# Kernel optimization log

Hardware: AMD Instinct MI355X
Metric: run time of the kernel (lower is better)

## Reference

```python
import jax, jax.numpy as jnp
import numpy as np

B, T, D, H = 2, 2048, 1024, 16
DH = D // H


def setup_inputs() -> dict:
    key = jax.random.key(0)
    ks = jax.random.split(key, 11)
    s = 1.0 / np.sqrt(D)
    return {
        "q": jax.random.normal(ks[0], (B, T, D), jnp.float32),
        "k": jax.random.normal(ks[1], (B, T, D), jnp.float32),
        "v": jax.random.normal(ks[2], (B, T, D), jnp.float32),
        "wq_w": jax.random.normal(ks[3], (D, D), jnp.float32) * s,
        "wq_b": jnp.zeros((D,), jnp.float32),
        "wk_w": jax.random.normal(ks[4], (D, D), jnp.float32) * s,
        "wk_b": jnp.zeros((D,), jnp.float32),
        "wv_w": jax.random.normal(ks[5], (D, D), jnp.float32) * s,
        "wv_b": jnp.zeros((D,), jnp.float32),
        "wo_w": jax.random.normal(ks[6], (D, D), jnp.float32) * s,
        "wo_b": jnp.zeros((D,), jnp.float32),
    }


def reference(q, k, v, wq_w, wq_b, wk_w, wk_b, wv_w, wv_b, wo_w, wo_b):
    b, t, d = q.shape
    # Linear projections (torch Linear: x @ W^T + b)
    wq = (q @ wq_w.T + wq_b).reshape(b, t, H, DH)
    wk = (k @ wk_w.T + wk_b).reshape(b, t, H, DH)
    wv = (v @ wv_w.T + wv_b).reshape(b, t, H, DH)
    # scaled dot-product attention: [b,h,t,s]
    scores = jnp.einsum('bthd,bshd->bhts', wq, wk) / jnp.sqrt(jnp.float32(DH))
    probs = jax.nn.softmax(scores, axis=-1)
    attn = jnp.einsum('bhts,bshd->bthd', probs, wv)  # [b,t,h,dh]
    attn = attn.reshape(b, t, d)
    return attn @ wo_w.T + wo_b
```

## Files before the change

kernel.cpp:

```cpp
#include <hip/hip_runtime.h>
#include <hip/hip_bf16.h>
#include <stdint.h>

#define Bn  2
#define Tn  2048
#define Dn  1024
#define Hn  16
#define DHn 64
#define Mn  (Bn*Tn)

typedef __attribute__((ext_vector_type(8))) short short8;
typedef __attribute__((ext_vector_type(4))) short short4v;
typedef __attribute__((ext_vector_type(4))) float f32x4;

__device__ __forceinline__ f32x4 fzero4() { f32x4 z = {0.f, 0.f, 0.f, 0.f}; return z; }

#define TR16(dst, a32) asm volatile("ds_read_b64_tr_b16 %0, %1" : "=v"(dst) : "v"(a32))
#define EXP2(x) __builtin_amdgcn_exp2f(x)

__device__ __forceinline__ short8 cvt8(const float4& a, const float4& b) {
    union { __hip_bfloat16 h[8]; short8 u; } w;
    w.h[0] = __float2bfloat16(a.x); w.h[1] = __float2bfloat16(a.y);
    w.h[2] = __float2bfloat16(a.z); w.h[3] = __float2bfloat16(a.w);
    w.h[4] = __float2bfloat16(b.x); w.h[5] = __float2bfloat16(b.y);
    w.h[6] = __float2bfloat16(b.z); w.h[7] = __float2bfloat16(b.w);
    return w.u;
}

__global__ void cvt3_kernel(const float* __restrict__ a0, const float* __restrict__ a1,
                            const float* __restrict__ a2,
                            __hip_bfloat16* __restrict__ o0, __hip_bfloat16* __restrict__ o1,
                            __hip_bfloat16* __restrict__ o2, int n)
{
    const int i = (blockIdx.x * blockDim.x + threadIdx.x) * 8;
    if (i >= n) return;
    const float* in = blockIdx.y == 0 ? a0 : (blockIdx.y == 1 ? a1 : a2);
    __hip_bfloat16* out = blockIdx.y == 0 ? o0 : (blockIdx.y == 1 ? o1 : o2);
    float4 a = *(const float4*)(in + i);
    float4 b = *(const float4*)(in + i + 4);
    *(short8*)(out + i) = cvt8(a, b);
}

__global__ __launch_bounds__(256, 3)
void gemm_qkv_kernel(const float* __restrict__ qa, const float* __restrict__ ka,
                     const float* __restrict__ va,
                     const __hip_bfloat16* __restrict__ wq, const __hip_bfloat16* __restrict__ wk,
                     const __hip_bfloat16* __restrict__ wv,
                     const float* __restrict__ bq_, const float* __restrict__ bk_,
                     const float* __restrict__ bv_,
                     __hip_bfloat16* __restrict__ Qp, __hip_bfloat16* __restrict__ Kp,
                     __hip_bfloat16* __restrict__ Vp)
{
    __shared__ alignas(16) short As[2][128*32];
    __shared__ alignas(16) short Bs[2][128*32];
    const int grp = blockIdx.y >> 3;
    const float* A           = grp == 0 ? qa : (grp == 1 ? ka : va);
    const __hip_bfloat16* Bw = grp == 0 ? wq : (grp == 1 ? wk : wv);
    const float* bias        = grp == 0 ? bq_ : (grp == 1 ? bk_ : bv_);
    __hip_bfloat16* C        = grp == 0 ? Qp : (grp == 1 ? Kp : Vp);
    const float scl          = grp == 0 ? 0.18033688011112042f : 1.0f;

    const int t = threadIdx.x, lane = t & 63, wave = t >> 6;
    const int wm = wave >> 1, wn = wave & 1;
    const int row0 = blockIdx.x * 128, col0 = (blockIdx.y & 7) * 128;

    f32x4 acc[4][4];
#pragma unroll
    for (int m = 0; m < 4; ++m)
#pragma unroll
        for (int n = 0; n < 4; ++n) acc[m][n] = fzero4();

    const int srow = wave*16 + (lane >> 2);
    const int skk  = (lane & 3) * 8;
    const int ldsb = wave * 1024 + (lane & 63) * 16;

    float4 ra[2][2];
    auto LOAD_A = [&](int k0) {
#pragma unroll
        for (int i = 0; i < 2; ++i) {
            const float* ap = A + (size_t)(row0 + i*64 + srow)*Dn + k0 + skk;
            ra[i][0] = *(const float4*)ap;
            ra[i][1] = *(const float4*)(ap + 4);
        }
    };
    auto WRITE_A = [&](int buf) {
#pragma unroll
        for (int i = 0; i < 2; ++i)
            *(short8*)((char*)As[buf] + i*4096 + ldsb) = cvt8(ra[i][0], ra[i][1]);
    };
    auto STAGE_B = [&](int buf, int k0) {
#pragma unroll
        for (int i = 0; i < 2; ++i)
            __builtin_amdgcn_global_load_lds(
                (const __attribute__((address_space(1))) void*)(Bw + (size_t)(col0 + i*64 + srow)*Dn + k0 + skk),
                (__attribute__((address_space(3))) void*)((char*)Bs[buf] + i*4096 + wave*1024 + (lane&63)*16), 16, 0, 0);
    };

    LOAD_A(0);
    STAGE_B(0, 0);
    WRITE_A(0);
    __syncthreads();
    int cur = 0;
    for (int k0 = 0; k0 < Dn; k0 += 32) {
        const bool more = (k0 + 32 < Dn);
        if (more) { LOAD_A(k0 + 32); STAGE_B(cur ^ 1, k0 + 32); }
        short8 af[4], bf_[4];
#pragma unroll
        for (int m = 0; m < 4; ++m)
            af[m] = *(const short8*)((char*)As[cur] + (wm*64 + m*16 + (lane & 15))*64 + (lane >> 4)*16);
#pragma unroll
        for (int n = 0; n < 4; ++n)
            bf_[n] = *(const short8*)((char*)Bs[cur] + (wn*64 + n*16 + (lane & 15))*64 + (lane >> 4)*16);
        __builtin_amdgcn_s_setprio(1);
#pragma unroll
        for (int m = 0; m < 4; ++m)
#pragma unroll
            for (int n = 0; n < 4; ++n)
                acc[m][n] = __builtin_amdgcn_mfma_f32_16x16x32_bf16(af[m], bf_[n], acc[m][n], 0, 0, 0);
        __builtin_amdgcn_s_setprio(0);
        __builtin_amdgcn_sched_barrier(0);
        if (more) WRITE_A(cur ^ 1);
        __syncthreads();
        cur ^= 1;
    }

#pragma unroll
    for (int n = 0; n < 4; ++n) {
        const int col = col0 + wn*64 + n*16 + (lane & 15);
        const float bv = bias[col];
#pragma unroll
        for (int m = 0; m < 4; ++m) {
            const int rb_ = row0 + wm*64 + m*16 + (lane>>4)*4;
#pragma unroll
            for (int i = 0; i < 4; ++i)
                C[(size_t)(rb_+i)*Dn + col] = __float2bfloat16((acc[m][n][i] + bv) * scl);
        }
    }
}

__global__ __launch_bounds__(256, 4)
void gemm_out_kernel(const __hip_bfloat16* __restrict__ A,
                     const __hip_bfloat16* __restrict__ Bw,
                     const float* __restrict__ bias,
                     float* __restrict__ C)
{
    __shared__ alignas(16) short As[2][64*32];
    __shared__ alignas(16) short Bs[2][128*32];
    const int t = threadIdx.x, lane = t & 63, wave = t >> 6;
    const int wm = wave >> 1, wn = wave & 1;
    const int row0 = blockIdx.x * 64, col0 = blockIdx.y * 128;

    f32x4 acc[2][4];
#pragma unroll
    for (int m = 0; m < 2; ++m)
#pragma unroll
        for (int n = 0; n < 4; ++n) acc[m][n] = fzero4();

    const int srow = wave*16 + (lane >> 2);
    const int skk  = (lane & 3) * 8;
    const int ldsb = wave * 1024;

    auto STAGE = [&](int buf, int k0) {
        __builtin_amdgcn_global_load_lds(
            (const __attribute__((address_space(1))) void*)(A + (size_t)(row0 + srow)*Dn + k0 + skk),
            (__attribute__((address_space(3))) void*)((char*)As[buf] + ldsb), 16, 0, 0);
#pragma unroll
        for (int i = 0; i < 2; ++i)
            __builtin_amdgcn_global_load_lds(
                (const __attribute__((address_space(1))) void*)(Bw + (size_t)(col0 + i*64 + srow)*Dn + k0 + skk),
                (__attribute__((address_space(3))) void*)((char*)Bs[buf] + i*4096 + ldsb), 16, 0, 0);
    };

    STAGE(0, 0);
    __syncthreads();
    int cur = 0;
    for (int k0 = 0; k0 < Dn; k0 += 32) {
        if (k0 + 32 < Dn) STAGE(cur ^ 1, k0 + 32);
        short8 af[2], bf_[4];
#pragma unroll
        for (int m = 0; m < 2; ++m)
            af[m] = *(const short8*)((char*)As[cur] + (wm*32 + m*16 + (lane & 15))*64 + (lane >> 4)*16);
#pragma unroll
        for (int n = 0; n < 4; ++n)
            bf_[n] = *(const short8*)((char*)Bs[cur] + (wn*64 + n*16 + (lane & 15))*64 + (lane >> 4)*16);
        __builtin_amdgcn_s_setprio(1);
#pragma unroll
        for (int m = 0; m < 2; ++m)
#pragma unroll
            for (int n = 0; n < 4; ++n)
                acc[m][n] = __builtin_amdgcn_mfma_f32_16x16x32_bf16(af[m], bf_[n], acc[m][n], 0, 0, 0);
        __builtin_amdgcn_s_setprio(0);
        __syncthreads();
        cur ^= 1;
    }

#pragma unroll
    for (int n = 0; n < 4; ++n) {
        const int col = col0 + wn*64 + n*16 + (lane & 15);
        const float bv = bias[col];
#pragma unroll
        for (int m = 0; m < 2; ++m) {
            const int rb_ = row0 + wm*32 + m*16 + (lane>>4)*4;
#pragma unroll
            for (int i = 0; i < 4; ++i)
                C[(size_t)(rb_+i)*Dn + col] = acc[m][n][i] + bv;
        }
    }
}

#define VPL 1288

__global__ __launch_bounds__(256, 2)
void attn_kernel(const __hip_bfloat16* __restrict__ Q,
                 const __hip_bfloat16* __restrict__ K,
                 const __hip_bfloat16* __restrict__ V,
                 __hip_bfloat16* __restrict__ O,
                 const float* __restrict__ wo_src,
                 __hip_bfloat16* __restrict__ wo_dst)
{
    __shared__ alignas(16) short Vlds[2*2*4*VPL];
    const int t = threadIdx.x, lane = t & 63, wave = t >> 6;

    {
        const int off = (blockIdx.x * 256 + t) * 8;
        float4 a = *(const float4*)(wo_src + off);
        float4 b2 = *(const float4*)(wo_src + off + 4);
        *(short8*)(wo_dst + off) = cvt8(a, b2);
    }

    const int g = lane >> 4, c = lane & 15;
    const int pk = wave & 1, qh = wave >> 1;
    const int blk = (blockIdx.x & 7) * 64 + (blockIdx.x >> 3);
    const int qb = blk & 15;
    const int h  = (blk >> 4) & (Hn - 1);
    const int b  = blk >> 8;
    const size_t base = (size_t)b * Tn * Dn + (size_t)h * DHn;
    const int q0 = qb * 128 + qh * 64;

    short8 bq[4][2];
#pragma unroll
    for (int qs = 0; qs < 4; ++qs) {
        const __hip_bfloat16* qp = Q + base + (size_t)(q0 + qs*16 + c) * Dn + g*8;
        bq[qs][0] = *(const short8*)qp;
        bq[qs][1] = *(const short8*)(qp + 32);
    }
    short8 ones;
#pragma unroll
    for (int i = 0; i < 8; ++i) ones[i] = (short)0x3F80;

    f32x4 o_[4][4];
#pragma unroll
    for (int qs = 0; qs < 4; ++qs)
#pragma unroll
        for (int d = 0; d < 4; ++d) o_[qs][d] = fzero4();
    float m_[4] = {-3e38f, -3e38f, -3e38f, -3e38f};
    f32x4 lacc[4] = {fzero4(), fzero4(), fzero4(), fzero4()};

    const int vrow = t >> 3;
    const int vd0  = ((t>>1)&3)*VPL + (vrow>>2)*80 + (vrow&3)*16 + (t&1)*8;
    const int vcol = (((t>>1)&3)*16 + (t&1)*8);
    const uint32_t vbase = (uint32_t)(uintptr_t)(void*)Vlds;
    const uint32_t atr = vbase + (uint32_t)(pk*10304 + g*160 + c*8);

    short8 akA[4][2], akB[4][2];
    {
        const __hip_bfloat16* kp = K + base + (size_t)(pk*64 + c) * Dn + g*8;
#pragma unroll
        for (int sub = 0; sub < 4; ++sub)
#pragma unroll
            for (int ks = 0; ks < 2; ++ks)
                akA[sub][ks] = *(const short8*)(kp + (size_t)sub*16*Dn + ks*32);
    }

    auto ITER = [&](const short8 (&ck)[4][2], short8 (&nk)[4][2], int it) {
        const int kv0 = it * 128;
        short8 cv[2][2];
#pragma unroll
        for (int p = 0; p < 2; ++p) {
            const __hip_bfloat16* vp = V + base + (size_t)(kv0 + p*64 + vrow) * Dn + vcol;
            cv[p][0] = *(const short8*)vp;
            cv[p][1] = *(const short8*)(vp + (size_t)32*Dn);
        }
        {
            const int kvn = (it < 15) ? kv0 + 128 + pk*64 : pk*64;
            const __hip_bfloat16* kp = K + base + (size_t)(kvn + c) * Dn + g*8;
#pragma unroll
            for (int sub = 0; sub < 4; ++sub)
#pragma unroll
                for (int ks = 0; ks < 2; ++ks)
                    nk[sub][ks] = *(const short8*)(kp + (size_t)sub*16*Dn + ks*32);
        }

        short8 pa[4][2];
#pragma unroll
        for (int qs = 0; qs < 4; ++qs) {
            f32x4 s_[4];
#pragma unroll
            for (int sub = 0; sub < 4; ++sub) s_[sub] = fzero4();
            __builtin_amdgcn_s_setprio(1);
#pragma unroll
            for (int sub = 0; sub < 4; ++sub)
#pragma unroll
                for (int ks = 0; ks < 2; ++ks)
                    s_[sub] = __builtin_amdgcn_mfma_f32_16x16x32_bf16(
                        ck[sub][ks], bq[qs][ks], s_[sub], 0, 0, 0);
            __builtin_amdgcn_s_setprio(0);

            float r0 = fmaxf(fmaxf(s_[0][0], s_[0][1]), fmaxf(s_[0][2], s_[0][3]));
            float r1 = fmaxf(fmaxf(s_[1][0], s_[1][1]), fmaxf(s_[1][2], s_[1][3]));
            float r2 = fmaxf(fmaxf(s_[2][0], s_[2][1]), fmaxf(s_[2][2], s_[2][3]));
            float r3 = fmaxf(fmaxf(s_[3][0], s_[3][1]), fmaxf(s_[3][2], s_[3][3]));
            float rm = fmaxf(fmaxf(r0, r1), fmaxf(r2, r3));
            if (!__all(rm - m_[qs] <= 8.0f)) {
                float gm = fmaxf(rm, __shfl_xor(rm, 16));
                gm = fmaxf(gm, __shfl_xor(gm, 32));
                const float mn = fmaxf(m_[qs], gm);
                const float sc = EXP2(m_[qs] - mn);
                m_[qs] = mn;
                lacc[qs][0] *= sc;
#pragma unroll
                for (int d = 0; d < 4; ++d)
#pragma unroll
                    for (int i = 0; i < 4; ++i) o_[qs][d][i] *= sc;
            }
            const float mn = m_[qs];
#pragma unroll
            for (int kc = 0; kc < 2; ++kc)
#pragma unroll
                for (int hf = 0; hf < 2; ++hf)
#pragma unroll
                    for (int i = 0; i < 4; ++i) {
                        const float p = EXP2(s_[kc*2+hf][i] - mn);
                        union { __hip_bfloat16 hb; short u; } cvp;
                        cvp.hb = __float2bfloat16(p);
                        pa[qs][kc][hf*4 + i] = cvp.u;
                    }
            lacc[qs] = __builtin_amdgcn_mfma_f32_16x16x32_bf16(ones, pa[qs][0], lacc[qs], 0, 0, 0);
            lacc[qs] = __builtin_amdgcn_mfma_f32_16x16x32_bf16(ones, pa[qs][1], lacc[qs], 0, 0, 0);
        }

        short* vb = Vlds + (it & 1) * 10304;
#pragma unroll
        for (int p = 0; p < 2; ++p) {
            *(short8*)(vb + p*5152 + vd0)       = cv[p][0];
            *(short8*)(vb + p*5152 + vd0 + 640) = cv[p][1];
        }
        asm volatile("s_waitcnt lgkmcnt(0)" ::: "memory");
        __builtin_amdgcn_s_barrier();
        __builtin_amdgcn_sched_barrier(0);

        const uint32_t atrb = atr + (uint32_t)((it & 1) * 20608u);
        short4v tv[4][2][2];
#pragma unroll
        for (int d = 0; d < 4; ++d)
#pragma unroll
            for (int kc = 0; kc < 2; ++kc) {
                const uint32_t a = atrb + (uint32_t)(d*2576 + kc*1280);
                TR16(tv[d][kc][0], a);
                TR16(tv[d][kc][1], a + 640);
            }
#pragma unroll
        for (int d = 0; d < 4; ++d) {
            if (d == 0)      asm volatile("s_waitcnt lgkmcnt(12)" ::: "memory");
            else if (d == 1) asm volatile("s_waitcnt lgkmcnt(8)" ::: "memory");
            else if (d == 2) asm volatile("s_waitcnt lgkmcnt(4)" ::: "memory");
            else             asm volatile("s_waitcnt lgkmcnt(0)" ::: "memory");
            __builtin_amdgcn_sched_barrier(0);
            const short8 av0 = __builtin_shufflevector(tv[d][0][0], tv[d][0][1], 0,1,2,3,4,5,6,7);
            const short8 av1 = __builtin_shufflevector(tv[d][1][0], tv[d][1][1], 0,1,2,3,4,5,6,7);
            __builtin_amdgcn_s_setprio(1);
#pragma unroll
            for (int qs = 0; qs < 4; ++qs) {
                o_[qs][d] = __builtin_amdgcn_mfma_f32_16x16x32_bf16(av0, pa[qs][0], o_[qs][d], 0, 0, 0);
                o_[qs][d] = __builtin_amdgcn_mfma_f32_16x16x32_bf16(av1, pa[qs][1], o_[qs][d], 0, 0, 0);
            }
            __builtin_amdgcn_s_setprio(0);
        }
    };

    for (int j = 0; j < 8; ++j) {
        ITER(akA, akB, 2*j);
        ITER(akB, akA, 2*j + 1);
    }

    __syncthreads();
    float* cbase = (float*)Vlds;
    if (pk == 1) {
        float* cb = cbase + qh * 4608;
#pragma unroll
        for (int qs = 0; qs < 4; ++qs)
#pragma unroll
            for (int d = 0; d < 4; ++d)
                *(f32x4*)(cb + ((qs*4 + d)*64 + lane)*4) = o_[qs][d];
#pragma unroll
        for (int qs = 0; qs < 4; ++qs) {
            cb[4096 + qs*64 + lane] = m_[qs];
            cb[4352 + qs*64 + lane] = lacc[qs][0];
        }
    }
    __syncthreads();
    if (pk == 0) {
        float* cb = cbase + qh * 4608;
#pragma unroll
        for (int qs = 0; qs < 4; ++qs) {
            const float m1 = cb[4096 + qs*64 + lane];
            const float l1 = cb[4352 + qs*64 + lane];
            const float mN = fmaxf(m_[qs], m1);
            const float sc0 = EXP2(m_[qs] - mN);
            const float sc1 = EXP2(m1 - mN);
            const float inv = 1.f / (lacc[qs][0]*sc0 + l1*sc1);
            __hip_bfloat16* op = O + base + (size_t)(q0 + qs*16 + c) * Dn + g*4;
#pragma unroll
            for (int d = 0; d < 4; ++d) {
                const f32x4 o1 = *(const f32x4*)(cb + ((qs*4 + d)*64 + lane)*4);
                union { __hip_bfloat16 hb[4]; ushort4 u4; } w;
#pragma unroll
                for (int i = 0; i < 4; ++i)
                    w.hb[i] = __float2bfloat16((o_[qs][d][i]*sc0 + o1[i]*sc1) * inv);
                *(ushort4*)(op + d*16) = w.u4;
            }
        }
    }
}

extern "C" void kernel_launch(void* const* d_in, const int* in_sizes, int n_in,
                              void* d_out, int out_size, void* d_ws, size_t ws_size,
                              hipStream_t stream)
{
    (void)in_sizes; (void)n_in; (void)out_size; (void)ws_size;
    const float* q    = (const float*)d_in[0];
    const float* k    = (const float*)d_in[1];
    const float* v    = (const float*)d_in[2];
    const float* wq_w = (const float*)d_in[3];
    const float* wq_b = (const float*)d_in[4];
    const float* wk_w = (const float*)d_in[5];
    const float* wk_b = (const float*)d_in[6];
    const float* wv_w = (const float*)d_in[7];
    const float* wv_b = (const float*)d_in[8];
    const float* wo_w = (const float*)d_in[9];
    const float* wo_b = (const float*)d_in[10];

    char* ws = (char*)d_ws;
    const size_t W  = (size_t)Dn * Dn * 2;
    const size_t S1 = (size_t)Mn * Dn * 2;
    __hip_bfloat16* wqb = (__hip_bfloat16*)(ws);
    __hip_bfloat16* wkb = (__hip_bfloat16*)(ws + W);
    __hip_bfloat16* wvb = (__hip_bfloat16*)(ws + 2*W);
    __hip_bfloat16* wob = (__hip_bfloat16*)(ws + 3*W);
    __hip_bfloat16* Qp  = (__hip_bfloat16*)(ws + 4*W);
    __hip_bfloat16* Kp  = (__hip_bfloat16*)(ws + 4*W + S1);
    __hip_bfloat16* Vp  = (__hip_bfloat16*)(ws + 4*W + 2*S1);
    __hip_bfloat16* Ap  = (__hip_bfloat16*)(ws + 4*W + 3*S1);

    const int nW = Dn * Dn;
    cvt3_kernel<<<dim3(nW/2048, 3), 256, 0, stream>>>(wq_w, wk_w, wv_w, wqb, wkb, wvb, nW);

    gemm_qkv_kernel<<<dim3(Mn/128, 24), 256, 0, stream>>>(
        q, k, v, wqb, wkb, wvb, wq_b, wk_b, wv_b, Qp, Kp, Vp);

    attn_kernel<<<Bn*Hn*(Tn/128), 256, 0, stream>>>(Qp, Kp, Vp, Ap, wo_w, wob);

    gemm_out_kernel<<<dim3(Mn/64, Dn/128), 256, 0, stream>>>(Ap, wob, wo_b, (float*)d_out);
}
```

Before: 120.8 us.

## Prefetch A two k-steps ahead in QKV GEMM with explicit vmcnt waits

Restructures the QKV projection GEMM main loop to load fp32 A tiles two iterations ahead using two register sets, unrolled by two. Each step writes the previous prefetch into the other LDS buffer and replaces __syncthreads with explicit s_waitcnt vmcnt(4) plus s_barrier, so in-flight global loads do not need to drain before each barrier. This is meant to hide global load latency for A behind the MFMA work. The cost is higher register pressure, and the hand-counted vmcnt values depend on the exact number of outstanding loads.

After: 124.4 us. 1.03x slower.

```diff
diff --git a/kernel.cpp b/kernel.cpp
--- a/kernel.cpp
+++ b/kernel.cpp
@@ -74,19 +74,19 @@
     const int skk  = (lane & 3) * 8;
     const int ldsb = wave * 1024 + (lane & 63) * 16;
 
-    float4 ra[2][2];
-    auto LOAD_A = [&](int k0) {
+    float4 raA[2][2], raB[2][2];
+    auto LOAD_A = [&](int k0, float4 (&r)[2][2]) {
 #pragma unroll
         for (int i = 0; i < 2; ++i) {
             const float* ap = A + (size_t)(row0 + i*64 + srow)*Dn + k0 + skk;
-            ra[i][0] = *(const float4*)ap;
-            ra[i][1] = *(const float4*)(ap + 4);
-        }
-    };
-    auto WRITE_A = [&](int buf) {
+            r[i][0] = *(const float4*)ap;
+            r[i][1] = *(const float4*)(ap + 4);
+        }
+    };
+    auto WRITE_A = [&](int buf, float4 (&r)[2][2]) {
 #pragma unroll
         for (int i = 0; i < 2; ++i)
-            *(short8*)((char*)As[buf] + i*4096 + ldsb) = cvt8(ra[i][0], ra[i][1]);
+            *(short8*)((char*)As[buf] + i*4096 + ldsb) = cvt8(r[i][0], r[i][1]);
     };
     auto STAGE_B = [&](int buf, int k0) {
 #pragma unroll
@@ -95,15 +95,7 @@
                 (const __attribute__((address_space(1))) void*)(Bw + (size_t)(col0 + i*64 + srow)*Dn + k0 + skk),
                 (__attribute__((address_space(3))) void*)((char*)Bs[buf] + i*4096 + wave*1024 + (lane&63)*16), 16, 0, 0);
     };
-
-    LOAD_A(0);
-    STAGE_B(0, 0);
-    WRITE_A(0);
-    __syncthreads();
-    int cur = 0;
-    for (int k0 = 0; k0 < Dn; k0 += 32) {
-        const bool more = (k0 + 32 < Dn);
-        if (more) { LOAD_A(k0 + 32); STAGE_B(cur ^ 1, k0 + 32); }
+    auto COMPUTE = [&](int cur) {
         short8 af[4], bf_[4];
 #pragma unroll
         for (int m = 0; m < 4; ++m)
@@ -119,9 +111,44 @@
                 acc[m][n] = __builtin_amdgcn_mfma_f32_16x16x32_bf16(af[m], bf_[n], acc[m][n], 0, 0, 0);
         __builtin_amdgcn_s_setprio(0);
         __builtin_amdgcn_sched_barrier(0);
-        if (more) WRITE_A(cur ^ 1);
-        __syncthreads();
-        cur ^= 1;
+    };
+
+    LOAD_A(0, raA);
+    STAGE_B(0, 0);
+    WRITE_A(0, raA);
+    LOAD_A(32, raB);
+    asm volatile("s_waitcnt vmcnt(4) lgkmcnt(0)" ::: "memory");
+    __builtin_amdgcn_s_barrier();
+
+    int cur = 0;
+    for (int j = 0; j < 16; ++j) {
+        {
+            const int k0 = j*64;
+            const bool more2 = (k0 + 64 < Dn);
+            STAGE_B(cur ^ 1, k0 + 32);
+            if (more2) LOAD_A(k0 + 64, raA);
+            COMPUTE(cur);
+            WRITE_A(cur ^ 1, raB);
+            if (more2) asm volatile("s_waitcnt vmcnt(4) lgkmcnt(0)" ::: "memory");
+            else       asm volatile("s_waitcnt vmcnt(0) lgkmcnt(0)" ::: "memory");
+            __builtin_amdgcn_s_barrier();
+            cur ^= 1;
+        }
+        {
+            const int k0 = j*64 + 32;
+            const bool more  = (k0 + 32 < Dn);
+            const bool more2 = (k0 + 64 < Dn);
+            if (more)  STAGE_B(cur ^ 1, k0 + 32);
+            if (more2) LOAD_A(k0 + 64, raB);
+            COMPUTE(cur);
+            if (more) {
+                WRITE_A(cur ^ 1, raA);
+                if (more2) asm volatile("s_waitcnt vmcnt(4) lgkmcnt(0)" ::: "memory");
+                else       asm volatile("s_waitcnt vmcnt(0) lgkmcnt(0)" ::: "memory");
+                __builtin_amdgcn_s_barrier();
+            }
+            cur ^= 1;
+        }
     }
 
 #pragma unroll
```
